# Kernel tuning notes

Hardware: AMD Instinct MI355X
Metric: run time of the kernel (lower is better)

## Reference

```python
import jax, jax.numpy as jnp
import numpy as np

H, DH, M = 8, 64, 3          # heads, dim_head, num memory tokens
DIM = 512                    # model dim
INNER = H * DH               # 512
SCALE = DH ** -0.5
SQRT_DH = float(np.sqrt(DH))
SQRT_M = float(np.sqrt(M))


def setup_inputs() -> dict:
    key = jax.random.key(0)
    ks = jax.random.split(key, 7)
    b, n = 2, 2048
    x = jax.random.normal(ks[0], (b, n, DIM), dtype=jnp.float32)
    # Linear weights stored as (in, out); y = x @ W
    wq = jax.random.normal(ks[1], (DIM, INNER), dtype=jnp.float32) * (DIM ** -0.5)
    wkv = jax.random.normal(ks[2], (DIM, 2 * INNER), dtype=jnp.float32) * (DIM ** -0.5)
    wo = jax.random.normal(ks[3], (INNER, DIM), dtype=jnp.float32) * (INNER ** -0.5)
    bo = jnp.zeros((DIM,), dtype=jnp.float32)
    # xavier_normal_ std = sqrt(2 / (fan_in + fan_out)) over last two dims (M, INNER)
    xav = float(np.sqrt(2.0 / (M + INNER)))
    m_k = jax.random.normal(ks[4], (1, M, INNER), dtype=jnp.float32) * xav
    m_v = jax.random.normal(ks[5], (1, M, INNER), dtype=jnp.float32) * xav
    return {"x": x, "wq": wq, "wkv": wkv, "wo": wo, "bo": bo, "m_k": m_k, "m_v": m_v}


def reference(x, wq, wkv, wo, bo, m_k, m_v):
    b, n, _ = x.shape
    # projections -> (b, h, n, d)
    q = (x @ wq).reshape(b, n, H, DH).transpose(0, 2, 1, 3)
    kv = x @ wkv
    k, v = jnp.split(kv, 2, axis=-1)
    k = k.reshape(b, n, H, DH).transpose(0, 2, 1, 3)
    v = v.reshape(b, n, H, DH).transpose(0, 2, 1, 3)
    # memory tokens: torch does expand(b, M, INNER).view(b, H, M, DH),
    # a flat reshape (NOT a per-head rearrange) -- replicate exactly.
    mk = SQRT_DH * jnp.broadcast_to(m_k, (b, M, INNER)).reshape(b, H, M, DH)
    mv = SQRT_M * jnp.broadcast_to(m_v, (b, M, INNER)).reshape(b, H, M, DH)
    k = jnp.concatenate([k, mk], axis=2)  # (b, h, n+M, d)
    v = jnp.concatenate([v, mv], axis=2)
    dots = jnp.einsum('bhid,bhjd->bhij', q, k) * SCALE  # (b, h, n, n+M)
    attn = jax.nn.softmax(dots, axis=-1)                # dropout = identity (eval)
    out = jnp.einsum('bhij,bhjd->bhid', attn, v)
    out = out.transpose(0, 2, 1, 3).reshape(b, n, INNER)
    return out @ wo + bo
```

## Files before the change

kernel.cpp:

```cpp
#include <hip/hip_runtime.h>

typedef unsigned short u16;
typedef __attribute__((ext_vector_type(8))) __bf16 bf16x8;
typedef __attribute__((ext_vector_type(4))) float f32x4;

#define DEVI __device__ __forceinline__

#define NEG_BIG (-30000.0f)
#define SMAX 16.0f

DEVI float bf2f(u16 u) {
    unsigned int v = ((unsigned int)u) << 16;
    return __uint_as_float(v);
}
DEVI u16 f2bf(float f) {
    unsigned int x = __float_as_uint(f);
    x += 0x7fffu + ((x >> 16) & 1u);
    return (u16)(x >> 16);
}
DEVI bf16x8 ldb8(const u16* p) {
    union { uint4 u; bf16x8 b; } c;
    c.u = *(const uint4*)p;
    return c.b;
}
DEVI f32x4 mfma32(bf16x8 a, bf16x8 b, f32x4 c) {
    return __builtin_amdgcn_mfma_f32_16x16x32_bf16(a, b, c, 0, 0, 0);
}
DEVI float clamp4(float v) {
    return fminf(fmaxf(v, -1e4f), 1e4f);
}

__global__ __launch_bounds__(256) void prep(
    const float* __restrict__ wq, const float* __restrict__ wkv,
    const float* __restrict__ wo, const float* __restrict__ x,
    u16* __restrict__ wqkvT, u16* __restrict__ woT, u16* __restrict__ xb)
{
    const int bid = blockIdx.x, tid = threadIdx.x;
    if (bid < 256) {
        __shared__ u16 T[64][68];
        int j0, k0; const float* W; int ldw; u16* Out;
        if (bid < 192) { int jt = bid % 24, kt = bid / 24;
            j0 = jt * 64; k0 = kt * 64;
            if (j0 < 512) { W = wq + j0;        ldw = 512;  }
            else          { W = wkv + (j0-512); ldw = 1024; }
            Out = wqkvT;
        } else { int t = bid - 192;
            j0 = (t >> 3) * 64; k0 = (t & 7) * 64;
            W = wo + j0; ldw = 512; Out = woT;
        }
        const int lr = tid >> 4, lc = tid & 15;
        #pragma unroll
        for (int i = 0; i < 4; ++i) {
            int k = lr + i * 16;
            float4 v = *(const float4*)(W + (size_t)(k0 + k) * ldw + lc * 4);
            u16 p[4] = { f2bf(v.x), f2bf(v.y), f2bf(v.z), f2bf(v.w) };
            *(uint2*)&T[k][lc * 4] = *(uint2*)p;
        }
        __syncthreads();
        #pragma unroll
        for (int i = 0; i < 4; ++i) {
            int j = lr + i * 16;
            u16 p[4];
            #pragma unroll
            for (int c = 0; c < 4; ++c) p[c] = T[lc * 4 + c][j];
            *(uint2*)(Out + (size_t)(j0 + j) * 512 + k0 + lc * 4) = *(uint2*)p;
        }
    } else {
        int e = (bid - 256) * 1024 + tid * 4;
        float4 v = *(const float4*)(x + e);
        u16 p[4] = { f2bf(v.x), f2bf(v.y), f2bf(v.z), f2bf(v.w) };
        *(uint2*)(xb + e) = *(uint2*)p;
    }
}

template<bool F32OUT>
__global__ __launch_bounds__(256) void gemm_bt(
    const u16* __restrict__ A, int lda,
    const u16* __restrict__ BT, int ldb,
    void* __restrict__ Cv, int ldc,
    const float* __restrict__ bias, int K)
{
    __shared__ alignas(16) u16 As[64][40];
    __shared__ alignas(16) u16 Bs[64][40];

    const int tid = threadIdx.x;
    const int m0 = blockIdx.x * 64, n0 = blockIdx.y * 64;
    const int w = tid >> 6, lane = tid & 63, l15 = lane & 15, quad = lane >> 4;
    const int srow = tid >> 2, scg = (tid & 3) * 8;

    f32x4 acc[4];
    for (int t = 0; t < 4; ++t) acc[t] = (f32x4){0.f, 0.f, 0.f, 0.f};

    const uint4* ag = (const uint4*)(A + (size_t)(m0 + srow) * lda + scg);
    const uint4* bg = (const uint4*)(BT + (size_t)(n0 + srow) * ldb + scg);

    for (int k0 = 0; k0 < K; k0 += 32) {
        uint4 av = *ag; uint4 bv = *bg;
        ag += 4; bg += 4;
        __syncthreads();
        *(uint4*)&As[srow][scg] = av;
        *(uint4*)&Bs[srow][scg] = bv;
        __syncthreads();
        bf16x8 af = ldb8(&As[16 * w + l15][quad * 8]);
        #pragma unroll
        for (int t = 0; t < 4; ++t) {
            bf16x8 bf = ldb8(&Bs[16 * t + l15][quad * 8]);
            acc[t] = mfma32(af, bf, acc[t]);
        }
    }

    #pragma unroll
    for (int t = 0; t < 4; ++t) {
        int col = n0 + 16 * t + l15;
        float bv = bias ? bias[col] : 0.f;
        #pragma unroll
        for (int r = 0; r < 4; ++r) {
            int row = m0 + 16 * w + quad * 4 + r;
            float vr = clamp4(acc[t][r] + bv);
            if (F32OUT) ((float*)Cv)[(size_t)row * ldc + col] = vr;
            else        ((u16*)Cv)[(size_t)row * ldc + col] = f2bf(vr);
        }
    }
}

__global__ __launch_bounds__(256) void attn_kernel(
    const u16* __restrict__ qkv, const float* __restrict__ mkf,
    const float* __restrict__ mvf, float* __restrict__ Opart,
    float* __restrict__ Lpart)
{
    __shared__ alignas(16) u16 Ks[64][72];
    __shared__ alignas(16) u16 Vt[64][72];
    __shared__ alignas(16) u16 QP[64][72];

    const int tid = threadIdx.x;
    const int qt = blockIdx.x >> 1, s = blockIdx.x & 1;
    const int h = blockIdx.y, b = blockIdx.z;
    const int w = tid >> 6, lane = tid & 63, l15 = lane & 15, quad = lane >> 4;
    const int r0 = b * 2048 + qt * 64;

    {
        int row = tid >> 2, cg = (tid & 3) * 16;
        const u16* src = qkv + (size_t)(r0 + row) * 1536 + h * 64 + cg;
        #pragma unroll
        for (int i = 0; i < 16; ++i)
            QP[row][cg + i] = f2bf(bf2f(src[i]) * 0.125f);
    }
    __syncthreads();
    bf16x8 qf[2];
    qf[0] = ldb8(&QP[16 * w + l15][quad * 8]);
    qf[1] = ldb8(&QP[16 * w + l15][32 + quad * 8]);

    f32x4 O[4];
    for (int t = 0; t < 4; ++t) O[t] = (f32x4){0.f, 0.f, 0.f, 0.f};
    float l_lane[4] = {0.f, 0.f, 0.f, 0.f};

    const int krow = tid >> 2, kcg = (tid & 3) * 16;
    const int vkp = (tid & 31) * 2;
    const int vdg = ((tid >> 5) & 7) * 8;

    const int kt0 = s ? 16 : 0, kt1 = s ? 33 : 16;
    for (int kt = kt0; kt < kt1; ++kt) {
        __syncthreads();
        {
            int kidx = kt * 64 + krow;
            if (kidx < 2048) {
                const u16* src = qkv + (size_t)(b * 2048 + kidx) * 1536 + 512 + h * 64 + kcg;
                *(uint4*)&Ks[krow][kcg]     = *(const uint4*)src;
                *(uint4*)&Ks[krow][kcg + 8] = *(const uint4*)(src + 8);
            } else if (kidx < 2051) {
                int m = kidx - 2048;
                const float* src = mkf + h * 192 + m * 64 + kcg;
                #pragma unroll
                for (int i = 0; i < 16; ++i)
                    Ks[krow][kcg + i] = f2bf(src[i] * 8.0f);
            } else {
                #pragma unroll
                for (int i = 0; i < 16; ++i) Ks[krow][kcg + i] = 0;
            }
        }
        {
            u16 va[8], vb[8];
            #pragma unroll
            for (int kk = 0; kk < 2; ++kk) {
                int kidx = kt * 64 + vkp + kk;
                u16* dst = kk ? vb : va;
                if (kidx < 2048) {
                    const u16* src = qkv + (size_t)(b * 2048 + kidx) * 1536 + 1024 + h * 64 + vdg;
                    #pragma unroll
                    for (int i = 0; i < 8; ++i) dst[i] = src[i];
                } else if (kidx < 2051) {
                    const float* src = mvf + h * 192 + (kidx - 2048) * 64 + vdg;
                    #pragma unroll
                    for (int i = 0; i < 8; ++i)
                        dst[i] = f2bf(src[i] * 1.7320508f);
                } else {
                    #pragma unroll
                    for (int i = 0; i < 8; ++i) dst[i] = 0;
                }
            }
            #pragma unroll
            for (int i = 0; i < 8; ++i) {
                unsigned int pk = (unsigned int)va[i] | ((unsigned int)vb[i] << 16);
                *(unsigned int*)&Vt[vdg + i][vkp] = pk;
            }
        }
        __syncthreads();

        f32x4 d4[4];
        for (int t = 0; t < 4; ++t) d4[t] = (f32x4){0.f, 0.f, 0.f, 0.f};
        #pragma unroll
        for (int ks = 0; ks < 2; ++ks) {
            #pragma unroll
            for (int t = 0; t < 4; ++t) {
                bf16x8 bf = ldb8(&Ks[16 * t + l15][ks * 32 + quad * 8]);
                d4[t] = mfma32(qf[ks], bf, d4[t]);
            }
        }
        if (kt == 32) {
            #pragma unroll
            for (int t = 0; t < 4; ++t)
                if (16 * t + l15 >= 3)
                    d4[t] = (f32x4){NEG_BIG, NEG_BIG, NEG_BIG, NEG_BIG};
        }

        #pragma unroll
        for (int t = 0; t < 4; ++t) {
            #pragma unroll
            for (int r = 0; r < 4; ++r) {
                float p = __expf(d4[t][r] - SMAX);
                l_lane[r] += p;
                QP[16 * w + quad * 4 + r][16 * t + l15] = f2bf(p);
            }
        }
        __syncthreads();

        #pragma unroll
        for (int ks = 0; ks < 2; ++ks) {
            bf16x8 af = ldb8(&QP[16 * w + l15][ks * 32 + quad * 8]);
            #pragma unroll
            for (int dt = 0; dt < 4; ++dt) {
                bf16x8 bf = ldb8(&Vt[16 * dt + l15][ks * 32 + quad * 8]);
                O[dt] = mfma32(af, bf, O[dt]);
            }
        }
    }

    #pragma unroll
    for (int r = 0; r < 4; ++r) {
        #pragma unroll
        for (int off = 1; off < 16; off <<= 1)
            l_lane[r] += __shfl_xor(l_lane[r], off, 64);
    }
    float* Ob = Opart + (size_t)s * 4096 * 512;
    #pragma unroll
    for (int r = 0; r < 4; ++r) {
        int row = r0 + 16 * w + quad * 4 + r;
        #pragma unroll
        for (int dt = 0; dt < 4; ++dt) {
            int col = h * 64 + 16 * dt + l15;
            Ob[(size_t)row * 512 + col] = O[dt][r];
        }
        if (l15 == 0)
            Lpart[((size_t)s * 4096 + row) * 8 + h] = l_lane[r];
    }
}

__global__ __launch_bounds__(256) void merge_kernel(
    const float* __restrict__ Opart, const float* __restrict__ Lpart,
    u16* __restrict__ outp)
{
    int e = (blockIdx.x * 256 + threadIdx.x) * 4;
    int row = e >> 9, col = e & 511, h = col >> 6;
    float4 a = *(const float4*)(Opart + e);
    float4 c = *(const float4*)(Opart + 4096 * 512 + e);
    float l = Lpart[row * 8 + h] + Lpart[(4096 + row) * 8 + h];
    float rl = 1.0f / fmaxf(l, 1e-30f);
    u16 p[4] = { f2bf(clamp4((a.x + c.x) * rl)), f2bf(clamp4((a.y + c.y) * rl)),
                 f2bf(clamp4((a.z + c.z) * rl)), f2bf(clamp4((a.w + c.w) * rl)) };
    *(uint2*)(outp + e) = *(uint2*)p;
}

extern "C" void kernel_launch(void* const* d_in, const int* in_sizes, int n_in,
                              void* d_out, int out_size, void* d_ws, size_t ws_size,
                              hipStream_t stream)
{
    (void)in_sizes; (void)n_in; (void)out_size; (void)ws_size;
    const float* x   = (const float*)d_in[0];
    const float* wq  = (const float*)d_in[1];
    const float* wkv = (const float*)d_in[2];
    const float* wo  = (const float*)d_in[3];
    const float* bo  = (const float*)d_in[4];
    const float* mk  = (const float*)d_in[5];
    const float* mv  = (const float*)d_in[6];
    float* out = (float*)d_out;

    u16* wqkvT = (u16*)d_ws;
    u16* woT   = wqkvT + 1536 * 512;
    u16* xb    = woT + 512 * 512;
    u16* qkv   = xb + (size_t)4096 * 512;
    u16* outp  = qkv + (size_t)4096 * 1536;
    float* Opart = (float*)(outp + (size_t)4096 * 512);
    float* Lpart = Opart + (size_t)2 * 4096 * 512;

    prep<<<2304, 256, 0, stream>>>(wq, wkv, wo, x, wqkvT, woT, xb);
    gemm_bt<false><<<dim3(64, 24), 256, 0, stream>>>(xb, 512, wqkvT, 512,
                                                     qkv, 1536, nullptr, 512);
    attn_kernel<<<dim3(64, 8, 2), 256, 0, stream>>>(qkv, mk, mv, Opart, Lpart);
    merge_kernel<<<2048, 256, 0, stream>>>(Opart, Lpart, outp);
    gemm_bt<true><<<dim3(64, 8), 256, 0, stream>>>(outp, 512, woT, 512,
                                                   out, 512, bo, 512);
}
```

Before: 149.8 us.

## Split attention KV into five chunks, pre-pad memory tokens, bf16 partials, wider GEMM k-step

Memory tokens are now written into padded rows of the qkv buffer by the prep kernel, so the attention inner loop has no per-tile branches. The KV range is split five ways instead of two to raise parallelism, and the partial outputs are stored in bf16 to cut merge traffic. The QK product is computed transposed so P can be packed directly without a block-wide sync, the Q scale is folded into the exp, and the GEMM k-tile grows to 64. In exchange the merge reads five partials, there is more rounding from the bf16 partials, and the workspace layout is reorganised with aliasing of scratch buffers.

```diff
diff --git a/kernel.cpp b/kernel.cpp
--- a/kernel.cpp
+++ b/kernel.cpp
@@ -1,12 +1,11 @@
 #include <hip/hip_runtime.h>
 
 typedef unsigned short u16;
+typedef unsigned int u32;
 typedef __attribute__((ext_vector_type(8))) __bf16 bf16x8;
 typedef __attribute__((ext_vector_type(4))) float f32x4;
 
 #define DEVI __device__ __forceinline__
-
-#define NEG_BIG (-30000.0f)
 #define SMAX 16.0f
 
 DEVI float bf2f(u16 u) {
@@ -18,6 +17,11 @@
     x += 0x7fffu + ((x >> 16) & 1u);
     return (u16)(x >> 16);
 }
+DEVI u32 pk2(float lo, float hi) {
+    union { __bf16 b[2]; u32 u; } c;
+    c.b[0] = (__bf16)lo; c.b[1] = (__bf16)hi;
+    return c.u;
+}
 DEVI bf16x8 ldb8(const u16* p) {
     union { uint4 u; bf16x8 b; } c;
     c.u = *(const uint4*)p;
@@ -26,14 +30,14 @@
 DEVI f32x4 mfma32(bf16x8 a, bf16x8 b, f32x4 c) {
     return __builtin_amdgcn_mfma_f32_16x16x32_bf16(a, b, c, 0, 0, 0);
 }
-DEVI float clamp4(float v) {
-    return fminf(fmaxf(v, -1e4f), 1e4f);
-}
+DEVI float clamp4(float v) { return fminf(fmaxf(v, -1e4f), 1e4f); }
 
 __global__ __launch_bounds__(256) void prep(
     const float* __restrict__ wq, const float* __restrict__ wkv,
     const float* __restrict__ wo, const float* __restrict__ x,
-    u16* __restrict__ wqkvT, u16* __restrict__ woT, u16* __restrict__ xb)
+    const float* __restrict__ mkf, const float* __restrict__ mvf,
+    u16* __restrict__ wqkvT, u16* __restrict__ woT, u16* __restrict__ xb,
+    u16* __restrict__ qkv)
 {
     const int bid = blockIdx.x, tid = threadIdx.x;
     if (bid < 256) {
@@ -41,8 +45,8 @@
         int j0, k0; const float* W; int ldw; u16* Out;
         if (bid < 192) { int jt = bid % 24, kt = bid / 24;
             j0 = jt * 64; k0 = kt * 64;
-            if (j0 < 512) { W = wq + j0;        ldw = 512;  }
-            else          { W = wkv + (j0-512); ldw = 1024; }
+            if (j0 < 512) { W = wq + j0;          ldw = 512;  }
+            else          { W = wkv + (j0 - 512); ldw = 1024; }
             Out = wqkvT;
         } else { int t = bid - 192;
             j0 = (t >> 3) * 64; k0 = (t & 7) * 64;
@@ -65,11 +69,22 @@
             for (int c = 0; c < 4; ++c) p[c] = T[lc * 4 + c][j];
             *(uint2*)(Out + (size_t)(j0 + j) * 512 + k0 + lc * 4) = *(uint2*)p;
         }
-    } else {
+    } else if (bid < 2304) {
         int e = (bid - 256) * 1024 + tid * 4;
         float4 v = *(const float4*)(x + e);
         u16 p[4] = { f2bf(v.x), f2bf(v.y), f2bf(v.z), f2bf(v.w) };
         *(uint2*)(xb + e) = *(uint2*)p;
+    } else {
+        int e = (bid - 2304) * 256 + tid;
+        int b = e >> 16, rem = e & 65535;
+        int row2 = rem >> 10, c = rem & 1023;
+        float v = 0.f;
+        if (row2 < 3) {
+            int hh = (c & 511) >> 6, d = c & 63;
+            int src = hh * 192 + row2 * 64 + d;
+            v = (c < 512) ? 8.0f * mkf[src] : 1.7320508f * mvf[src];
+        }
+        qkv[((size_t)b * 2112 + 2048 + row2) * 1536 + 512 + c] = f2bf(v);
     }
 }
 
@@ -78,34 +93,40 @@
     const u16* __restrict__ A, int lda,
     const u16* __restrict__ BT, int ldb,
     void* __restrict__ Cv, int ldc,
-    const float* __restrict__ bias, int K)
-{
-    __shared__ alignas(16) u16 As[64][40];
-    __shared__ alignas(16) u16 Bs[64][40];
+    const float* __restrict__ bias, int K, int mpad)
+{
+    __shared__ alignas(16) u16 As[64][72];
+    __shared__ alignas(16) u16 Bs[64][72];
 
     const int tid = threadIdx.x;
     const int m0 = blockIdx.x * 64, n0 = blockIdx.y * 64;
     const int w = tid >> 6, lane = tid & 63, l15 = lane & 15, quad = lane >> 4;
-    const int srow = tid >> 2, scg = (tid & 3) * 8;
+    const int srow = tid >> 2, scg = (tid & 3) * 16;
 
     f32x4 acc[4];
     for (int t = 0; t < 4; ++t) acc[t] = (f32x4){0.f, 0.f, 0.f, 0.f};
 
-    const uint4* ag = (const uint4*)(A + (size_t)(m0 + srow) * lda + scg);
-    const uint4* bg = (const uint4*)(BT + (size_t)(n0 + srow) * ldb + scg);
-
-    for (int k0 = 0; k0 < K; k0 += 32) {
-        uint4 av = *ag; uint4 bv = *bg;
-        ag += 4; bg += 4;
-        __syncthreads();
-        *(uint4*)&As[srow][scg] = av;
-        *(uint4*)&Bs[srow][scg] = bv;
-        __syncthreads();
-        bf16x8 af = ldb8(&As[16 * w + l15][quad * 8]);
-        #pragma unroll
-        for (int t = 0; t < 4; ++t) {
-            bf16x8 bf = ldb8(&Bs[16 * t + l15][quad * 8]);
-            acc[t] = mfma32(af, bf, acc[t]);
+    const u16* ap = A + (size_t)(m0 + srow) * lda + scg;
+    const u16* bp = BT + (size_t)(n0 + srow) * ldb + scg;
+
+    for (int k0 = 0; k0 < K; k0 += 64) {
+        uint4 a0 = *(const uint4*)ap, a1 = *(const uint4*)(ap + 8);
+        uint4 b0 = *(const uint4*)bp, b1 = *(const uint4*)(bp + 8);
+        ap += 64; bp += 64;
+        __syncthreads();
+        *(uint4*)&As[srow][scg]     = a0;
+        *(uint4*)&As[srow][scg + 8] = a1;
+        *(uint4*)&Bs[srow][scg]     = b0;
+        *(uint4*)&Bs[srow][scg + 8] = b1;
+        __syncthreads();
+        #pragma unroll
+        for (int ks = 0; ks < 2; ++ks) {
+            bf16x8 af = ldb8(&As[16 * w + l15][ks * 32 + quad * 8]);
+            #pragma unroll
+            for (int t = 0; t < 4; ++t) {
+                bf16x8 bf = ldb8(&Bs[16 * t + l15][ks * 32 + quad * 8]);
+                acc[t] = mfma32(af, bf, acc[t]);
+            }
         }
     }
 
@@ -116,92 +137,68 @@
         #pragma unroll
         for (int r = 0; r < 4; ++r) {
             int row = m0 + 16 * w + quad * 4 + r;
+            int orow = row + ((row >> 11) * mpad);
             float vr = clamp4(acc[t][r] + bv);
-            if (F32OUT) ((float*)Cv)[(size_t)row * ldc + col] = vr;
-            else        ((u16*)Cv)[(size_t)row * ldc + col] = f2bf(vr);
-        }
-    }
-}
-
-__global__ __launch_bounds__(256) void attn_kernel(
-    const u16* __restrict__ qkv, const float* __restrict__ mkf,
-    const float* __restrict__ mvf, float* __restrict__ Opart,
+            if (F32OUT) ((float*)Cv)[(size_t)orow * ldc + col] = vr;
+            else        ((u16*)Cv)[(size_t)orow * ldc + col] = f2bf(vr);
+        }
+    }
+}
+
+__global__ __launch_bounds__(256, 5) void attn_kernel(
+    const u16* __restrict__ qkv, u16* __restrict__ Opart,
     float* __restrict__ Lpart)
 {
     __shared__ alignas(16) u16 Ks[64][72];
     __shared__ alignas(16) u16 Vt[64][72];
-    __shared__ alignas(16) u16 QP[64][72];
+    __shared__ alignas(16) u16 Ps[64][72];
 
     const int tid = threadIdx.x;
-    const int qt = blockIdx.x >> 1, s = blockIdx.x & 1;
+    const int bx = blockIdx.x;
+    const int qt = bx / 5, s = bx - qt * 5;
     const int h = blockIdx.y, b = blockIdx.z;
     const int w = tid >> 6, lane = tid & 63, l15 = lane & 15, quad = lane >> 4;
-    const int r0 = b * 2048 + qt * 64;
+    const size_t bq = (size_t)b * 2112;
+    const int rq = qt * 64;
+    const int ro = b * 2048 + qt * 64;
 
     {
         int row = tid >> 2, cg = (tid & 3) * 16;
-        const u16* src = qkv + (size_t)(r0 + row) * 1536 + h * 64 + cg;
-        #pragma unroll
-        for (int i = 0; i < 16; ++i)
-            QP[row][cg + i] = f2bf(bf2f(src[i]) * 0.125f);
+        const u16* src = qkv + (bq + rq + row) * 1536 + h * 64 + cg;
+        *(uint4*)&Ks[row][cg]     = *(const uint4*)src;
+        *(uint4*)&Ks[row][cg + 8] = *(const uint4*)(src + 8);
     }
     __syncthreads();
     bf16x8 qf[2];
-    qf[0] = ldb8(&QP[16 * w + l15][quad * 8]);
-    qf[1] = ldb8(&QP[16 * w + l15][32 + quad * 8]);
+    qf[0] = ldb8(&Ks[16 * w + l15][quad * 8]);
+    qf[1] = ldb8(&Ks[16 * w + l15][32 + quad * 8]);
 
     f32x4 O[4];
     for (int t = 0; t < 4; ++t) O[t] = (f32x4){0.f, 0.f, 0.f, 0.f};
-    float l_lane[4] = {0.f, 0.f, 0.f, 0.f};
+    float l_lane = 0.f;
 
     const int krow = tid >> 2, kcg = (tid & 3) * 16;
-    const int vkp = (tid & 31) * 2;
-    const int vdg = ((tid >> 5) & 7) * 8;
-
-    const int kt0 = s ? 16 : 0, kt1 = s ? 33 : 16;
+    const int vkp = (tid & 31) * 2, vdg = ((tid >> 5) & 7) * 8;
+
+    const int kt0 = 7 * s - (s > 3 ? s - 3 : 0);
+    const int kt1 = kt0 + (s < 3 ? 7 : 6);
     for (int kt = kt0; kt < kt1; ++kt) {
         __syncthreads();
+        const u16* ksrc = qkv + (bq + kt * 64 + krow) * 1536 + 512 + h * 64 + kcg;
+        uint4 k0 = *(const uint4*)ksrc, k1 = *(const uint4*)(ksrc + 8);
+        const u16* vsrc = qkv + (bq + kt * 64 + vkp) * 1536 + 1024 + h * 64 + vdg;
+        uint4 v0 = *(const uint4*)vsrc, v1 = *(const uint4*)(vsrc + 1536);
+        *(uint4*)&Ks[krow][kcg]     = k0;
+        *(uint4*)&Ks[krow][kcg + 8] = k1;
         {
-            int kidx = kt * 64 + krow;
-            if (kidx < 2048) {
-                const u16* src = qkv + (size_t)(b * 2048 + kidx) * 1536 + 512 + h * 64 + kcg;
-                *(uint4*)&Ks[krow][kcg]     = *(const uint4*)src;
-                *(uint4*)&Ks[krow][kcg + 8] = *(const uint4*)(src + 8);
-            } else if (kidx < 2051) {
-                int m = kidx - 2048;
-                const float* src = mkf + h * 192 + m * 64 + kcg;
-                #pragma unroll
-                for (int i = 0; i < 16; ++i)
-                    Ks[krow][kcg + i] = f2bf(src[i] * 8.0f);
-            } else {
-                #pragma unroll
-                for (int i = 0; i < 16; ++i) Ks[krow][kcg + i] = 0;
-            }
-        }
-        {
-            u16 va[8], vb[8];
-            #pragma unroll
-            for (int kk = 0; kk < 2; ++kk) {
-                int kidx = kt * 64 + vkp + kk;
-                u16* dst = kk ? vb : va;
-                if (kidx < 2048) {
-                    const u16* src = qkv + (size_t)(b * 2048 + kidx) * 1536 + 1024 + h * 64 + vdg;
-                    #pragma unroll
-                    for (int i = 0; i < 8; ++i) dst[i] = src[i];
-                } else if (kidx < 2051) {
-                    const float* src = mvf + h * 192 + (kidx - 2048) * 64 + vdg;
-                    #pragma unroll
-                    for (int i = 0; i < 8; ++i)
-                        dst[i] = f2bf(src[i] * 1.7320508f);
-                } else {
-                    #pragma unroll
-                    for (int i = 0; i < 8; ++i) dst[i] = 0;
-                }
-            }
-            #pragma unroll
-            for (int i = 0; i < 8; ++i) {
-                unsigned int pk = (unsigned int)va[i] | ((unsigned int)vb[i] << 16);
-                *(unsigned int*)&Vt[vdg + i][vkp] = pk;
+            u32 a0[4] = {v0.x, v0.y, v0.z, v0.w};
+            u32 a1[4] = {v1.x, v1.y, v1.z, v1.w};
+            #pragma unroll
+            for (int i = 0; i < 4; ++i) {
+                u32 lo = __builtin_amdgcn_perm(a1[i], a0[i], 0x05040100u);
+                u32 hi = __builtin_amdgcn_perm(a1[i], a0[i], 0x07060302u);
+                *(u32*)&Vt[vdg + 2 * i][vkp]     = lo;
+                *(u32*)&Vt[vdg + 2 * i + 1][vkp] = hi;
             }
         }
         __syncthreads();
@@ -212,71 +209,71 @@
         for (int ks = 0; ks < 2; ++ks) {
             #pragma unroll
             for (int t = 0; t < 4; ++t) {
-                bf16x8 bf = ldb8(&Ks[16 * t + l15][ks * 32 + quad * 8]);
-                d4[t] = mfma32(qf[ks], bf, d4[t]);
+                bf16x8 kf = ldb8(&Ks[16 * t + l15][ks * 32 + quad * 8]);
+                d4[t] = mfma32(kf, qf[ks], d4[t]);
             }
         }
         if (kt == 32) {
             #pragma unroll
-            for (int t = 0; t < 4; ++t)
-                if (16 * t + l15 >= 3)
-                    d4[t] = (f32x4){NEG_BIG, NEG_BIG, NEG_BIG, NEG_BIG};
+            for (int t = 1; t < 4; ++t)
+                d4[t] = (f32x4){-1e9f, -1e9f, -1e9f, -1e9f};
+            #pragma unroll
+            for (int r = 0; r < 4; ++r)
+                if (!(quad == 0 && r < 3)) d4[0][r] = -1e9f;
         }
 
         #pragma unroll
         for (int t = 0; t < 4; ++t) {
-            #pragma unroll
-            for (int r = 0; r < 4; ++r) {
-                float p = __expf(d4[t][r] - SMAX);
-                l_lane[r] += p;
-                QP[16 * w + quad * 4 + r][16 * t + l15] = f2bf(p);
+            float p0 = __expf(fmaf(d4[t][0], 0.125f, -SMAX));
+            float p1 = __expf(fmaf(d4[t][1], 0.125f, -SMAX));
+            float p2 = __expf(fmaf(d4[t][2], 0.125f, -SMAX));
+            float p3 = __expf(fmaf(d4[t][3], 0.125f, -SMAX));
+            l_lane += (p0 + p1) + (p2 + p3);
+            uint2 pv = { pk2(p0, p1), pk2(p2, p3) };
+            *(uint2*)&Ps[16 * w + l15][16 * t + 4 * quad] = pv;
+        }
+        #pragma unroll
+        for (int ks = 0; ks < 2; ++ks) {
+            bf16x8 af = ldb8(&Ps[16 * w + l15][ks * 32 + quad * 8]);
+            #pragma unroll
+            for (int dt = 0; dt < 4; ++dt) {
+                bf16x8 vf = ldb8(&Vt[16 * dt + l15][ks * 32 + quad * 8]);
+                O[dt] = mfma32(af, vf, O[dt]);
             }
         }
-        __syncthreads();
-
-        #pragma unroll
-        for (int ks = 0; ks < 2; ++ks) {
-            bf16x8 af = ldb8(&QP[16 * w + l15][ks * 32 + quad * 8]);
-            #pragma unroll
-            for (int dt = 0; dt < 4; ++dt) {
-                bf16x8 bf = ldb8(&Vt[16 * dt + l15][ks * 32 + quad * 8]);
-                O[dt] = mfma32(af, bf, O[dt]);
-            }
-        }
-    }
-
+    }
+
+    l_lane += __shfl_xor(l_lane, 16, 64);
+    l_lane += __shfl_xor(l_lane, 32, 64);
+    u16* Ob = Opart + (size_t)s * 4096 * 512;
     #pragma unroll
     for (int r = 0; r < 4; ++r) {
-        #pragma unroll
-        for (int off = 1; off < 16; off <<= 1)
-            l_lane[r] += __shfl_xor(l_lane[r], off, 64);
-    }
-    float* Ob = Opart + (size_t)s * 4096 * 512;
+        int row = ro + 16 * w + quad * 4 + r;
+        #pragma unroll
+        for (int dt = 0; dt < 4; ++dt)
+            Ob[(size_t)row * 512 + h * 64 + 16 * dt + l15] = f2bf(O[dt][r]);
+    }
+    if (lane < 16)
+        Lpart[((size_t)s * 4096 + ro + 16 * w + lane) * 8 + h] = l_lane;
+}
+
+__global__ __launch_bounds__(256) void merge_kernel(
+    const u16* __restrict__ Opart, const float* __restrict__ Lpart,
+    u16* __restrict__ outp)
+{
+    int e = (blockIdx.x * 256 + threadIdx.x) * 4;
+    int row = e >> 9, h = (e & 511) >> 6;
+    float ax = 0.f, ay = 0.f, az = 0.f, aw = 0.f, l = 0.f;
     #pragma unroll
-    for (int r = 0; r < 4; ++r) {
-        int row = r0 + 16 * w + quad * 4 + r;
-        #pragma unroll
-        for (int dt = 0; dt < 4; ++dt) {
-            int col = h * 64 + 16 * dt + l15;
-            Ob[(size_t)row * 512 + col] = O[dt][r];
-        }
-        if (l15 == 0)
-            Lpart[((size_t)s * 4096 + row) * 8 + h] = l_lane[r];
-    }
-}
-
-__global__ __launch_bounds__(256) void merge_kernel(
-    const float* __restrict__ Opart, const float* __restrict__ Lpart,
-    u16* __restrict__ outp)
-{
-    int e = (blockIdx.x * 256 + threadIdx.x) * 4;
-    int row = e >> 9, col = e & 511, h = col >> 6;
-    float4 a = *(const float4*)(Opart + e);
-    float4 c = *(const float4*)(Opart + 4096 * 512 + e);
-    float l = Lpart[row * 8 + h] + Lpart[(4096 + row) * 8 + h];
+    for (int s = 0; s < 5; ++s) {
+        uint2 pv = *(const uint2*)(Opart + (size_t)s * 4096 * 512 + e);
+        ax += bf2f((u16)(pv.x & 0xffff)); ay += bf2f((u16)(pv.x >> 16));
+        az += bf2f((u16)(pv.y & 0xffff)); aw += bf2f((u16)(pv.y >> 16));
+        l += Lpart[((size_t)s * 4096 + row) * 8 + h];
+    }
     float rl = 1.0f / fmaxf(l, 1e-30f);
-    u16 p[4] = { f2bf(clamp4((a.x + c.x) * rl)), f2bf(clamp4((a.y + c.y) * rl)),
-                 f2bf(clamp4((a.z + c.z) * rl)), f2bf(clamp4((a.w + c.w) * rl)) };
+    u16 p[4] = { f2bf(clamp4(ax * rl)), f2bf(clamp4(ay * rl)),
+                 f2bf(clamp4(az * rl)), f2bf(clamp4(aw * rl)) };
     *(uint2*)(outp + e) = *(uint2*)p;
 }
 
@@ -294,19 +291,20 @@
     const float* mv  = (const float*)d_in[6];
     float* out = (float*)d_out;
 
-    u16* wqkvT = (u16*)d_ws;
-    u16* woT   = wqkvT + 1536 * 512;
-    u16* xb    = woT + 512 * 512;
-    u16* qkv   = xb + (size_t)4096 * 512;
-    u16* outp  = qkv + (size_t)4096 * 1536;
-    float* Opart = (float*)(outp + (size_t)4096 * 512);
-    float* Lpart = Opart + (size_t)2 * 4096 * 512;
-
-    prep<<<2304, 256, 0, stream>>>(wq, wkv, wo, x, wqkvT, woT, xb);
+    u16* qkv   = (u16*)d_ws;
+    u16* outp  = qkv + 6488064;
+    u16* woT   = outp + 2097152;
+    float* Lpart = (float*)(woT + 262144);
+    u16* scratch = (u16*)(Lpart + 163840);
+    u16* wqkvT = scratch;
+    u16* xb    = scratch + 786432;
+    u16* Opart = scratch;
+
+    prep<<<2816, 256, 0, stream>>>(wq, wkv, wo, x, mk, mv, wqkvT, woT, xb, qkv);
     gemm_bt<false><<<dim3(64, 24), 256, 0, stream>>>(xb, 512, wqkvT, 512,
-                                                     qkv, 1536, nullptr, 512);
-    attn_kernel<<<dim3(64, 8, 2), 256, 0, stream>>>(qkv, mk, mv, Opart, Lpart);
+                                                     qkv, 1536, nullptr, 512, 64);
+    attn_kernel<<<dim3(160, 8, 2), 256, 0, stream>>>(qkv, Opart, Lpart);
     merge_kernel<<<2048, 256, 0, stream>>>(Opart, Lpart, outp);
     gemm_bt<true><<<dim3(64, 8), 256, 0, stream>>>(outp, 512, woT, 512,
-                                                   out, 512, bo, 512);
-}
+                                                   out, 512, bo, 512, 0);
+}
```

After: 142.2 us. 5.1% less time.
